# Kernel tuning notes

Hardware: AMD Instinct MI355X
Metric: run time of the kernel (lower is better)

Reference implementation:

```python
import jax, jax.numpy as jnp
import numpy as np

NUM_EMBEDDINGS = 1024
EMBEDDING_DIM = 64
COMMITMENT_COST = 0.25
EPS = 1e-12  # F.normalize clamp eps


def _l2_normalize(v):
    n = jnp.linalg.norm(v, axis=-1, keepdims=True)
    return v / jnp.maximum(n, EPS)


def setup_inputs() -> dict:
    key = jax.random.key(0)
    k_x, k_w = jax.random.split(key)
    x = jax.random.normal(k_x, (262144, EMBEDDING_DIM), dtype=jnp.float32)
    # nn.init.uniform_(weight, -1/K, 1/K)
    lim = 1.0 / NUM_EMBEDDINGS
    codebook = jax.random.uniform(k_w, (NUM_EMBEDDINGS, EMBEDDING_DIM),
                                  minval=-lim, maxval=lim, dtype=jnp.float32)
    return {"x": x, "codebook": codebook}


def reference(x, codebook):
    # Normalized vectors used only for nearest-neighbor search.
    xn = _l2_normalize(x)                      # [N, D]
    cn = _l2_normalize(codebook)               # [K, D]
    # ||xn||^2 + ||cn||^2 - 2 xn.cn  -> [N, K]
    distances = (jnp.sum(xn * xn, axis=1, keepdims=True)
                 + jnp.sum(cn * cn, axis=1)
                 - 2.0 * jnp.einsum('nd,kd->nk', xn, cn))
    encoding_indices = jnp.argmin(distances, axis=1)           # [N]
    quantized_unnormalized = codebook[encoding_indices]        # [N, D]
    sg = jax.lax.stop_gradient
    codebook_loss = jnp.mean((quantized_unnormalized - sg(x)) ** 2)
    commitment_loss = jnp.mean((x - sg(quantized_unnormalized)) ** 2)
    quantized_ste = x + sg(quantized_unnormalized - x)
    return quantized_ste, codebook_loss, commitment_loss, encoding_indices
```

## Files before the change

### kernel.cpp

```cpp
#include <hip/hip_runtime.h>
#include <math.h>

#define EPS 1e-12f
constexpr int N_ROWS = 262144;
constexpr int KCODES = 1024;
constexpr int DIM    = 64;
constexpr int CHUNK_SH = 4096;
constexpr int TIE_THR = 15;

typedef __attribute__((ext_vector_type(8)))  short  short8;
typedef __attribute__((ext_vector_type(16))) float  float16;

__device__ inline unsigned short f2bf(float f) {
    unsigned int u = __float_as_uint(f);
    u = u + 0x7fff + ((u >> 16) & 1);
    return (unsigned short)(u >> 16);
}
__device__ inline float bf2f(unsigned short s) {
    return __uint_as_float(((unsigned int)s) << 16);
}

__global__ __launch_bounds__(64)
void vq_prep(const float* __restrict__ cb, float* __restrict__ cnT,
             float* __restrict__ cc, unsigned short* __restrict__ frag,
             float* __restrict__ dloss) {
    int n = blockIdx.x;
    int d = threadIdx.x;
    float v = cb[n * DIM + d];
    float s = v * v;
    #pragma unroll
    for (int off = 32; off; off >>= 1) s += __shfl_xor(s, off, 64);
    float vn = v / fmaxf(sqrtf(s), EPS);
    cnT[d * KCODES + n] = vn;
    float s2 = vn * vn;
    #pragma unroll
    for (int off = 32; off; off >>= 1) s2 += __shfl_xor(s2, off, 64);
    if (d == 0) cc[n] = s2;
    unsigned short hi = f2bf(vn);
    unsigned short lo = f2bf(vn - bf2f(hi));
    int g = n >> 5;
    int lane = (n & 31) + 32 * ((d >> 3) & 1);
    int si = d >> 4, j = d & 7;
    size_t base = (size_t)((g * 4 + si) * 2) * 512 + lane * 8 + j;
    frag[base]       = hi;
    frag[base + 512] = lo;
    if (n == 0 && d == 0) *dloss = 0.f;
}

__global__ __launch_bounds__(256, 2)
void vq_mfma(const float* __restrict__ x, const unsigned short* __restrict__ frag,
             const float* __restrict__ cb, const float* __restrict__ cnT,
             const float* __restrict__ cc, float* __restrict__ out_q,
             float* __restrict__ out_idx, float* __restrict__ partial,
             float* __restrict__ dloss) {
    __shared__ unsigned short Blds[2][CHUNK_SH];
    __shared__ int   ridx[128];
    __shared__ int   blist[128];
    __shared__ int   bcnt;
    __shared__ float redl[4];

    const int tid = threadIdx.x;
    const int w = tid >> 6, l = tid & 63;
    const int lc = l & 31, h = l >> 5;
    const int row0 = blockIdx.x * 128;

    if (tid == 0) bcnt = 0;

    short8 ahi[4], alo[4];
    {
        int row = row0 + w * 32 + lc;
        float xv[4][8]; float ss = 0.f;
        #pragma unroll
        for (int s = 0; s < 4; ++s) {
            const float* p = x + (size_t)row * DIM + s * 16 + h * 8;
            float4 a = *(const float4*)p;
            float4 b = *(const float4*)(p + 4);
            xv[s][0]=a.x; xv[s][1]=a.y; xv[s][2]=a.z; xv[s][3]=a.w;
            xv[s][4]=b.x; xv[s][5]=b.y; xv[s][6]=b.z; xv[s][7]=b.w;
            ss += a.x*a.x + a.y*a.y + a.z*a.z + a.w*a.w
                + b.x*b.x + b.y*b.y + b.z*b.z + b.w*b.w;
        }
        ss += __shfl_xor(ss, 32, 64);
        float inv = 1.0f / fmaxf(sqrtf(ss), EPS);
        #pragma unroll
        for (int s = 0; s < 4; ++s)
            #pragma unroll
            for (int j = 0; j < 8; ++j) {
                float v = xv[s][j] * inv;
                unsigned short hb = f2bf(v);
                unsigned short lb = f2bf(v - bf2f(hb));
                ahi[s][j] = (short)hb;
                alo[s][j] = (short)lb;
            }
    }

    int m1[16], m2[16];
    #pragma unroll
    for (int r = 0; r < 16; ++r) { m1[r] = 0; m2[r] = 0; }

    {
        const unsigned short* g = frag + (w * 2) * 512 + l * 8;
        #pragma unroll
        for (int q = 0; q < 2; ++q)
            __builtin_amdgcn_global_load_lds(
                (const __attribute__((address_space(1))) unsigned int*)(g + q * 512),
                (__attribute__((address_space(3))) unsigned int*)&Blds[0][(w * 2 + q) * 512],
                16, 0, 0);
    }

    for (int c = 0; c < 32; ++c) {
        __syncthreads();
        if (c < 31) {
            const unsigned short* g = frag + (size_t)(c + 1) * CHUNK_SH + (w * 2) * 512 + l * 8;
            #pragma unroll
            for (int q = 0; q < 2; ++q)
                __builtin_amdgcn_global_load_lds(
                    (const __attribute__((address_space(1))) unsigned int*)(g + q * 512),
                    (__attribute__((address_space(3))) unsigned int*)&Blds[(c + 1) & 1][(w * 2 + q) * 512],
                    16, 0, 0);
        }
        const unsigned short* B = Blds[c & 1];
        short8 bhi[4], blo[4];
        #pragma unroll
        for (int s = 0; s < 4; ++s) {
            bhi[s] = *((const short8*)&B[(s * 2    ) * 512] + l);
            blo[s] = *((const short8*)&B[(s * 2 + 1) * 512] + l);
        }
        float16 acc;
        #pragma unroll
        for (int r = 0; r < 16; ++r) acc[r] = 2.0f;
        #pragma unroll
        for (int s = 0; s < 4; ++s) {
            acc = __builtin_amdgcn_mfma_f32_32x32x16_bf16(ahi[s], bhi[s], acc, 0, 0, 0);
            acc = __builtin_amdgcn_mfma_f32_32x32x16_bf16(alo[s], bhi[s], acc, 0, 0, 0);
            acc = __builtin_amdgcn_mfma_f32_32x32x16_bf16(ahi[s], blo[s], acc, 0, 0, 0);
        }
        #pragma unroll
        for (int r = 0; r < 16; ++r) {
            int k = (__float_as_int(acc[r]) & (int)0xFFFFFFE0) | c;
            int nm2;
            asm("v_med3_i32 %0, %1, %2, %3"
                : "=v"(nm2) : "v"(m1[r]), "v"(m2[r]), "v"(k));
            m2[r] = nm2;
            m1[r] = max(m1[r], k);
        }
    }

    #pragma unroll
    for (int r = 0; r < 16; ++r) {
        int a = m1[r], b = m2[r];
        #pragma unroll
        for (int off = 1; off < 32; off <<= 1) {
            int oa = __shfl_xor(a, off, 64);
            int ob = __shfl_xor(b, off, 64);
            int nb = max(max(b, ob), min(a, oa));
            a = max(a, oa); b = nb;
        }
        unsigned long long ball = __ballot(m1[r] == a);
        unsigned m32 = h ? (unsigned)(ball >> 32) : (unsigned)ball;
        if (lc == 0) {
            int rowl = w * 32 + (r & 3) + 8 * (r >> 2) + 4 * h;
            int wlc = 31 - __builtin_clz(m32);
            ridx[rowl] = (a & 31) * 32 + wlc;
            if (((a >> 5) - (b >> 5)) <= TIE_THR) {
                int p = atomicAdd(&bcnt, 1);
                if (p < 128) blist[p] = rowl;
            }
        }
    }
    __syncthreads();

    if (tid < 128) out_idx[row0 + tid] = (float)ridx[tid];

    float lsum = 0.f;
    const float4* cb4 = (const float4*)cb;
    const float4* x4  = (const float4*)x;
    float4*       o4  = (float4*)out_q;
    #pragma unroll
    for (int i = 0; i < 8; ++i) {
        int f = tid + 256 * i;
        int r = f >> 4, c4 = f & 15;
        float4 q  = cb4[ridx[r] * 16 + c4];
        float4 xr = x4[(size_t)row0 * 16 + f];
        o4[(size_t)row0 * 16 + f] = q;
        float dx = q.x - xr.x, dy = q.y - xr.y, dz = q.z - xr.z, dw = q.w - xr.w;
        lsum += dx * dx + dy * dy + dz * dz + dw * dw;
    }
    #pragma unroll
    for (int off = 32; off; off >>= 1) lsum += __shfl_xor(lsum, off, 64);
    if (l == 0) redl[w] = lsum;
    __syncthreads();
    if (tid == 0) partial[blockIdx.x] = redl[0] + redl[1] + redl[2] + redl[3];

    int nfl = bcnt; if (nfl > 128) nfl = 128;
    for (int e = w; e < nfl; e += 4) {
        int rowl = blist[e];
        int row  = row0 + rowl;
        float xl = x[(size_t)row * DIM + l];
        float ss = xl * xl;
        #pragma unroll
        for (int off = 32; off; off >>= 1) ss += __shfl_xor(ss, off, 64);
        float inv = 1.0f / fmaxf(sqrtf(ss), EPS);
        float dot[16];
        #pragma unroll
        for (int kk = 0; kk < 16; ++kk) dot[kk] = 0.f;
        for (int d = 0; d < 64; ++d) {
            float xd = __shfl(xl, d, 64);
            #pragma unroll
            for (int kk = 0; kk < 16; ++kk)
                dot[kk] = fmaf(xd, cnT[d * KCODES + l + 64 * kk], dot[kk]);
        }
        float best = INFINITY; int bix = 0x7fffffff;
        #pragma unroll
        for (int kk = 0; kk < 16; ++kk) {
            int k = l + 64 * kk;
            float dist = cc[k] - 2.0f * (inv * dot[kk]);
            if (dist < best) { best = dist; bix = k; }
        }
        #pragma unroll
        for (int off = 1; off < 64; off <<= 1) {
            float ob = __shfl_xor(best, off, 64);
            int   oi = __shfl_xor(bix,  off, 64);
            if (ob < best || (ob == best && oi < bix)) { best = ob; bix = oi; }
        }
        int oldi = ridx[rowl];
        if (bix != oldi) {
            float qn = cb[(size_t)bix  * DIM + l];
            float qo = cb[(size_t)oldi * DIM + l];
            float an = qn - xl, ao = qo - xl;
            float dl = an * an - ao * ao;
            #pragma unroll
            for (int off = 32; off; off >>= 1) dl += __shfl_xor(dl, off, 64);
            out_q[(size_t)row * DIM + l] = qn;
            if (l == 0) { out_idx[row] = (float)bix; atomicAdd(dloss, dl); }
        }
    }
}

__global__ __launch_bounds__(256)
void vq_final(const float* __restrict__ partial, const float* __restrict__ dloss,
              float* __restrict__ out_loss) {
    float s = 0.f;
    for (int i = threadIdx.x; i < 2048; i += 256) s += partial[i];
    #pragma unroll
    for (int off = 32; off; off >>= 1) s += __shfl_xor(s, off, 64);
    __shared__ float red[4];
    if ((threadIdx.x & 63) == 0) red[threadIdx.x >> 6] = s;
    __syncthreads();
    if (threadIdx.x == 0) {
        float t = red[0] + red[1] + red[2] + red[3] + *dloss;
        float m = t / (float)((size_t)N_ROWS * DIM);
        out_loss[0] = m;
        out_loss[1] = m;
    }
}

extern "C" void kernel_launch(void* const* d_in, const int* in_sizes, int n_in,
                              void* d_out, int out_size, void* d_ws, size_t ws_size,
                              hipStream_t stream) {
    const float* x  = (const float*)d_in[0];
    const float* cb = (const float*)d_in[1];
    float* out = (float*)d_out;
    float* out_q    = out;
    float* out_loss = out + (size_t)N_ROWS * DIM;
    float* out_idx  = out_loss + 2;

    char* ws = (char*)d_ws;
    float*          cnT     = (float*)(ws);
    float*          cc      = (float*)(ws + 262144);
    unsigned short* frag    = (unsigned short*)(ws + 266240);
    float*          dloss   = (float*)(ws + 528388);
    float*          partial = (float*)(ws + 790544);

    vq_prep <<<KCODES, 64, 0, stream>>>(cb, cnT, cc, frag, dloss);
    vq_mfma <<<N_ROWS / 128, 256, 0, stream>>>(x, frag, cb, cnT, cc,
                                               out_q, out_idx, partial, dloss);
    vq_final<<<1, 256, 0, stream>>>(partial, dloss, out_loss);
}
```

Measured before the change: 228.5 us.

## Load codebook fragments directly from global and fold final loss reduction into main kernel

Drops the LDS double-buffered async copy of codebook fragments and the per-chunk __syncthreads, so each wave reads its MFMA B operands straight from global memory (served by L2/L1, since every block reads the same 256KB). The separate final-reduction kernel is removed: each block atomically adds its loss partial to one accumulator, and the last block, found through an atomic done-counter, writes the mean loss. This cuts a kernel launch and block-level barriers, but adds global load latency inside the MFMA loop and makes the float loss sum depend on atomic ordering.

Result: slower. 308.1 us (+34.8%).

```diff
diff --git a/kernel.cpp b/kernel.cpp
--- a/kernel.cpp
+++ b/kernel.cpp
@@ -5,7 +5,6 @@
 constexpr int N_ROWS = 262144;
 constexpr int KCODES = 1024;
 constexpr int DIM    = 64;
-constexpr int CHUNK_SH = 4096;
 constexpr int TIE_THR = 15;
 
 typedef __attribute__((ext_vector_type(8)))  short  short8;
@@ -23,7 +22,7 @@
 __global__ __launch_bounds__(64)
 void vq_prep(const float* __restrict__ cb, float* __restrict__ cnT,
              float* __restrict__ cc, unsigned short* __restrict__ frag,
-             float* __restrict__ dloss) {
+             float* __restrict__ lossacc, int* __restrict__ donecnt) {
     int n = blockIdx.x;
     int d = threadIdx.x;
     float v = cb[n * DIM + d];
@@ -44,20 +43,20 @@
     size_t base = (size_t)((g * 4 + si) * 2) * 512 + lane * 8 + j;
     frag[base]       = hi;
     frag[base + 512] = lo;
-    if (n == 0 && d == 0) *dloss = 0.f;
+    if (n == 0 && d == 0) { *lossacc = 0.f; *donecnt = 0; }
 }
 
 __global__ __launch_bounds__(256, 2)
 void vq_mfma(const float* __restrict__ x, const unsigned short* __restrict__ frag,
              const float* __restrict__ cb, const float* __restrict__ cnT,
              const float* __restrict__ cc, float* __restrict__ out_q,
-             float* __restrict__ out_idx, float* __restrict__ partial,
-             float* __restrict__ dloss) {
-    __shared__ unsigned short Blds[2][CHUNK_SH];
+             float* __restrict__ out_idx, float* __restrict__ lossacc,
+             int* __restrict__ donecnt, float* __restrict__ out_loss) {
     __shared__ int   ridx[128];
     __shared__ int   blist[128];
     __shared__ int   bcnt;
     __shared__ float redl[4];
+    __shared__ int   lastflag;
 
     const int tid = threadIdx.x;
     const int w = tid >> 6, l = tid & 63;
@@ -98,33 +97,15 @@
     #pragma unroll
     for (int r = 0; r < 16; ++r) { m1[r] = 0; m2[r] = 0; }
 
-    {
-        const unsigned short* g = frag + (w * 2) * 512 + l * 8;
-        #pragma unroll
-        for (int q = 0; q < 2; ++q)
-            __builtin_amdgcn_global_load_lds(
-                (const __attribute__((address_space(1))) unsigned int*)(g + q * 512),
-                (__attribute__((address_space(3))) unsigned int*)&Blds[0][(w * 2 + q) * 512],
-                16, 0, 0);
-    }
-
-    for (int c = 0; c < 32; ++c) {
-        __syncthreads();
-        if (c < 31) {
-            const unsigned short* g = frag + (size_t)(c + 1) * CHUNK_SH + (w * 2) * 512 + l * 8;
-            #pragma unroll
-            for (int q = 0; q < 2; ++q)
-                __builtin_amdgcn_global_load_lds(
-                    (const __attribute__((address_space(1))) unsigned int*)(g + q * 512),
-                    (__attribute__((address_space(3))) unsigned int*)&Blds[(c + 1) & 1][(w * 2 + q) * 512],
-                    16, 0, 0);
-        }
-        const unsigned short* B = Blds[c & 1];
+    __syncthreads();
+
+    const short8* F = (const short8*)frag;
+    for (int g = 0; g < 32; ++g) {
         short8 bhi[4], blo[4];
         #pragma unroll
         for (int s = 0; s < 4; ++s) {
-            bhi[s] = *((const short8*)&B[(s * 2    ) * 512] + l);
-            blo[s] = *((const short8*)&B[(s * 2 + 1) * 512] + l);
+            bhi[s] = F[(size_t)((g * 4 + s) * 2    ) * 64 + l];
+            blo[s] = F[(size_t)((g * 4 + s) * 2 + 1) * 64 + l];
         }
         float16 acc;
         #pragma unroll
@@ -137,7 +118,7 @@
         }
         #pragma unroll
         for (int r = 0; r < 16; ++r) {
-            int k = (__float_as_int(acc[r]) & (int)0xFFFFFFE0) | c;
+            int k = (__float_as_int(acc[r]) & (int)0xFFFFFFE0) | g;
             int nm2;
             asm("v_med3_i32 %0, %1, %2, %3"
                 : "=v"(nm2) : "v"(m1[r]), "v"(m2[r]), "v"(k));
@@ -190,7 +171,7 @@
     for (int off = 32; off; off >>= 1) lsum += __shfl_xor(lsum, off, 64);
     if (l == 0) redl[w] = lsum;
     __syncthreads();
-    if (tid == 0) partial[blockIdx.x] = redl[0] + redl[1] + redl[2] + redl[3];
+    if (tid == 0) atomicAdd(lossacc, redl[0] + redl[1] + redl[2] + redl[3]);
 
     int nfl = bcnt; if (nfl > 128) nfl = 128;
     for (int e = w; e < nfl; e += 4) {
@@ -232,23 +213,19 @@
             #pragma unroll
             for (int off = 32; off; off >>= 1) dl += __shfl_xor(dl, off, 64);
             out_q[(size_t)row * DIM + l] = qn;
-            if (l == 0) { out_idx[row] = (float)bix; atomicAdd(dloss, dl); }
-        }
-    }
-}
-
-__global__ __launch_bounds__(256)
-void vq_final(const float* __restrict__ partial, const float* __restrict__ dloss,
-              float* __restrict__ out_loss) {
-    float s = 0.f;
-    for (int i = threadIdx.x; i < 2048; i += 256) s += partial[i];
-    #pragma unroll
-    for (int off = 32; off; off >>= 1) s += __shfl_xor(s, off, 64);
-    __shared__ float red[4];
-    if ((threadIdx.x & 63) == 0) red[threadIdx.x >> 6] = s;
-    __syncthreads();
-    if (threadIdx.x == 0) {
-        float t = red[0] + red[1] + red[2] + red[3] + *dloss;
+            if (l == 0) { out_idx[row] = (float)bix; atomicAdd(lossacc, dl); }
+        }
+    }
+
+    __syncthreads();
+    if (tid == 0) {
+        __threadfence();
+        int prev = atomicAdd(donecnt, 1);
+        lastflag = (prev == (int)gridDim.x - 1);
+    }
+    __syncthreads();
+    if (lastflag && tid == 0) {
+        float t = atomicAdd(lossacc, 0.0f);
         float m = t / (float)((size_t)N_ROWS * DIM);
         out_loss[0] = m;
         out_loss[1] = m;
@@ -269,11 +246,10 @@
     float*          cnT     = (float*)(ws);
     float*          cc      = (float*)(ws + 262144);
     unsigned short* frag    = (unsigned short*)(ws + 266240);
-    float*          dloss   = (float*)(ws + 528388);
-    float*          partial = (float*)(ws + 790544);
-
-    vq_prep <<<KCODES, 64, 0, stream>>>(cb, cnT, cc, frag, dloss);
+    float*          lossacc = (float*)(ws + 528384);
+    int*            donecnt = (int*)(ws + 528388);
+
+    vq_prep <<<KCODES, 64, 0, stream>>>(cb, cnT, cc, frag, lossacc, donecnt);
     vq_mfma <<<N_ROWS / 128, 256, 0, stream>>>(x, frag, cb, cnT, cc,
-                                               out_q, out_idx, partial, dloss);
-    vq_final<<<1, 256, 0, stream>>>(partial, dloss, out_loss);
-}
+                                               out_q, out_idx, lossacc, donecnt, out_loss);
+}
```
